# Optimization experiments

Measured on AMD Instinct MI355X. Metric: run time of the kernel, lower is better.

The kernel has to match this reference:

```python
import jax, jax.numpy as jnp
import numpy as np

EPS = 1e-5
AVG_D = 32.0


def setup_inputs() -> dict:
    key = jax.random.key(0)
    ks = jax.random.split(key, 12)
    Ns, Nd, E, D, K = 1_000_000, 100_000, 3_200_000, 16, 2
    Fs, Fd, V = 4, 4, 100_000
    F = Fd + K  # predictor fields
    inp = {}
    inp["Cat_src"] = jax.random.randint(ks[0], (Ns, Fs), 0, V)
    inp["Cat_dst"] = jax.random.randint(ks[1], (Nd, Fd), 0, V)
    inp["src_ids"] = jax.random.randint(ks[2], (E,), 0, Ns)
    inp["dst_ids"] = jax.random.randint(ks[3], (E,), 0, Nd)
    inp["label"] = jax.random.randint(ks[4], (Nd,), 0, 2)
    inp["w"] = jax.random.normal(ks[5], (V, D), dtype=jnp.float32) * 0.05
    inp["W_agg"] = jax.random.normal(ks[6], (K, 12 * D, D), dtype=jnp.float32) * 0.05
    inp["b_agg"] = jnp.zeros((K, D), jnp.float32)
    inp["w_lin"] = jax.random.normal(ks[7], (F * D,), dtype=jnp.float32) * 0.05
    inp["b_lin"] = jnp.zeros((1,), jnp.float32)
    inp["W1"] = jax.random.normal(ks[8], (F * D, 64), dtype=jnp.float32) * 0.05
    inp["b1"] = jnp.zeros((64,), jnp.float32)
    inp["W2"] = jax.random.normal(ks[9], (64, 32), dtype=jnp.float32) * 0.05
    inp["b2"] = jnp.zeros((32,), jnp.float32)
    inp["W3"] = jax.random.normal(ks[10], (32, 1), dtype=jnp.float32) * 0.05
    inp["b3"] = jnp.zeros((1,), jnp.float32)
    return inp


def reference(Cat_src, Cat_dst, src_ids, dst_ids, label, w, W_agg, b_agg,
              w_lin, b_lin, W1, b1, W2, b2, W3, b3):
    Nd = Cat_dst.shape[0]
    # --- node embedding: gather cat fields, RowEmb with modes [mean, max] -> [Ns, K, D]
    emb = w[Cat_src]                                      # [Ns, Fs, D]
    h_src = jnp.stack([emb.mean(1), emb.max(1)], axis=1)  # [Ns, K, D]
    # --- multi-aggregator message passing (copy_u + segment min/max/mean, std via mean of h^2)
    m = h_src[src_ids]                                    # [E, K, D]
    deg = jax.ops.segment_sum(jnp.ones(src_ids.shape, m.dtype), dst_ids, Nd)
    safe = jnp.maximum(deg, 1.0)[:, None, None]
    mean = jax.ops.segment_sum(m, dst_ids, Nd) / safe
    mean2 = jax.ops.segment_sum(m * m, dst_ids, Nd) / safe
    has = (deg > 0)[:, None, None]
    mn = jnp.where(has, jax.ops.segment_min(m, dst_ids, Nd), 0.0)
    mx = jnp.where(has, jax.ops.segment_max(m, dst_ids, Nd), 0.0)
    std = jnp.sqrt(jax.nn.relu(mean2 - mean * mean) + EPS)
    tmp = jnp.concatenate([mean, mn, mx, std], axis=-1)   # [Nd, K, 4D]
    # --- PNA degree scalers: identity / amplification / attenuation
    logd = jnp.log(deg + 1.0)
    log_avg = jnp.log(AVG_D + 1.0)
    amp = (logd / log_avg)[:, None, None]
    att = jnp.where(logd > 0, log_avg / jnp.maximum(logd, EPS), 0.0)[:, None, None]
    scaled = jnp.concatenate([tmp, tmp * amp, tmp * att], axis=-1)  # [Nd, K, 12D]
    mes = jnp.einsum('nkf,kfd->nkd', scaled, W_agg) + b_agg          # [Nd, K, D]
    # --- final block: concat dst cat embeddings with aggregated messages
    x = jnp.concatenate([w[Cat_dst], mes], axis=1)        # [Nd, F, D]
    # --- DeepFM predictor: linear + FM pairwise + deep MLP
    flat = x.reshape(Nd, -1)
    lin = flat @ w_lin + b_lin[0]
    s = x.sum(1)
    fm = 0.5 * ((s * s) - (x * x).sum(1)).sum(-1)
    h = jax.nn.relu(flat @ W1 + b1)
    h = jax.nn.relu(h @ W2 + b2)
    deep = (h @ W3 + b3)[:, 0]
    pred = jax.nn.sigmoid(lin + fm + deep)
    return (pred, label)
```

## Files before the change

### kernel.cpp

```cpp
#include <hip/hip_runtime.h>
#include <math.h>

#define EPSF 1e-5f
#define CAP  88
#define SBH  9
#define MAXSB 256
#define SBCAP 23552
#define TILE 4096
#define XPADS2 104
#define X2PADS 72
#define NPACK 14336

typedef __attribute__((ext_vector_type(8))) short short8;
typedef __attribute__((ext_vector_type(4))) float float4v;

__device__ inline unsigned f2bf_rne(float x) {
    unsigned u = __float_as_uint(x);
    u += 0x7FFF + ((u >> 16) & 1);
    return u >> 16;
}
__device__ inline short bf16_of(float x) { return (short)f2bf_rne(x); }
__device__ inline float bf2f_lo(unsigned hv) { return __uint_as_float(hv << 16); }
__device__ inline float bf2f_hi(unsigned hv) { return __uint_as_float(hv & 0xFFFF0000u); }
__device__ inline float bf2f_s(ushort s) { return __uint_as_float((unsigned)s << 16); }

__global__ __launch_bounds__(256) void setup_all(
    int* sbcursor, int nsb,
    const float* __restrict__ W_agg, const float* __restrict__ W1,
    const float* __restrict__ W2, ushort* __restrict__ wpack,
    const float* __restrict__ w, ushort* __restrict__ wb, int VD, int do_cast)
{
    int bid = blockIdx.x;
    if (bid == 0) {
        int i = threadIdx.x;
        if (i < nsb) sbcursor[i] = i * SBCAP;
        return;
    }
    if (bid == 1) {
        for (int it = threadIdx.x; it < 1792; it += 256) {
            if (it < 768) {
                int t_g = it >> 6; int rem = it & 63;
                int q = rem >> 4, col = rem & 15;
                int kvar = t_g / 6, t = t_g % 6;
                const float* src = W_agg + kvar * 3072 + (t * 32 + q * 8) * 16 + col;
                ushort* dst = wpack + (size_t)it * 8;
#pragma unroll
                for (int j = 0; j < 8; ++j) dst[j] = (ushort)f2bf_rne(src[j * 16]);
            } else if (it < 1536) {
                int i2 = it - 768;
                int t = i2 >> 8; int rem = i2 & 255;
                int q = rem >> 6, col = rem & 63;
                const float* src = W1 + (t * 32 + q * 8) * 64 + col;
                ushort* dst = wpack + 6144 + (size_t)i2 * 8;
#pragma unroll
                for (int j = 0; j < 8; ++j) dst[j] = (ushort)f2bf_rne(src[j * 64]);
            } else {
                int i2 = it - 1536;
                int t = i2 >> 7; int rem = i2 & 127;
                int q = rem >> 5, col = rem & 31;
                const float* src = W2 + (t * 32 + q * 8) * 32 + col;
                ushort* dst = wpack + 12288 + (size_t)i2 * 8;
#pragma unroll
                for (int j = 0; j < 8; ++j) dst[j] = (ushort)f2bf_rne(src[j * 32]);
            }
        }
        return;
    }
    if (!do_cast) return;
    int i4 = ((bid - 2) * 256 + threadIdx.x) * 4;
    if (i4 + 3 < VD) {
        float4 v = *(const float4*)(w + i4);
        ushort4 o;
        o.x = (ushort)f2bf_rne(v.x); o.y = (ushort)f2bf_rne(v.y);
        o.z = (ushort)f2bf_rne(v.z); o.w = (ushort)f2bf_rne(v.w);
        *(ushort4*)(wb + i4) = o;
    } else {
        for (int j = i4; j < VD; ++j) wb[j] = (ushort)f2bf_rne(w[j]);
    }
}

__global__ __launch_bounds__(256) void build_h(
    const int* __restrict__ Cat_src, const ushort* __restrict__ wb,
    unsigned* __restrict__ h, int Ns)
{
    int gid = blockIdx.x * 256 + threadIdx.x;
    int s = gid >> 4;
    if (s >= Ns) return;
    int lane = threadIdx.x & 63;
    int d = lane & 15;
    int c = Cat_src[s * 4 + (d & 3)];
    float vs = 0.f, vm = -INFINITY;
#pragma unroll
    for (int f = 0; f < 4; ++f) {
        int id = __shfl(c, (lane & 48) + f, 64);
        float a = bf2f_s(wb[id * 16 + d]);
        vs += a; vm = fmaxf(vm, a);
    }
    unsigned packed = f2bf_rne(vs * 0.25f) | (f2bf_rne(vm) << 16);
    __builtin_nontemporal_store(packed, &h[s * 16 + d]);
}

__global__ __launch_bounds__(256) void scatter_sb(
    const int* __restrict__ src_ids, const int* __restrict__ dst_ids,
    int* sbcursor, unsigned* __restrict__ pairs1, int E, int nsb)
{
    __shared__ int cnt[MAXSB];
    __shared__ int base[MAXSB];
    int tid = threadIdx.x;
    int t0 = blockIdx.x * TILE;
    for (int i = tid; i < nsb; i += 256) cnt[i] = 0;
    __syncthreads();
    int rank[TILE / 256];
#pragma unroll
    for (int j = 0; j < TILE / 256; ++j) {
        int e = t0 + j * 256 + tid;
        rank[j] = (e < E) ? atomicAdd(&cnt[dst_ids[e] >> SBH], 1) : 0;
    }
    __syncthreads();
    for (int i = tid; i < nsb; i += 256) {
        int c = cnt[i];
        base[i] = c ? atomicAdd(&sbcursor[i], c) : 0;
    }
    __syncthreads();
#pragma unroll
    for (int j = 0; j < TILE / 256; ++j) {
        int e = t0 + j * 256 + tid;
        if (e < E) {
            int d = dst_ids[e];
            int sb = d >> SBH;
            int idx = base[sb] + rank[j];
            if (idx < (sb + 1) * SBCAP)
                pairs1[idx] = ((unsigned)src_ids[e] << 9) | (unsigned)(d & 511);
        }
    }
}

__global__ __launch_bounds__(256) void scatter_fine2(
    const unsigned* __restrict__ pairs1, const int* __restrict__ sbcursor,
    unsigned* __restrict__ pairs2, int* __restrict__ deg, int Nd)
{
    __shared__ int ofs[256];
    int S = blockIdx.x >> 1, half = blockIdx.x & 1;
    int tid = threadIdx.x;
    int sbs = S * SBCAP;
    int sbe = sbcursor[S];
    if (sbe > sbs + SBCAP) sbe = sbs + SBCAP;
    ofs[tid] = 0;
    __syncthreads();
    for (int i = sbs + tid; i < sbe; i += 256) {
        unsigned p = __builtin_nontemporal_load(&pairs1[i]);
        int dl = (int)(p & 511u);
        if ((dl >> 8) == half) {
            int l = dl & 255;
            int sl = atomicAdd(&ofs[l], 1);
            if (sl < CAP)
                pairs2[(size_t)((S << 9) + dl) * CAP + sl] = p >> 9;
        }
    }
    __syncthreads();
    int gdst = (S << 9) + (half << 8) + tid;
    if (gdst < Nd) deg[gdst] = ofs[tid];
}

__device__ inline void emit_stats(float sum0, float sq0, float mn0, float mx0,
                                  float sum1, float sq1, float mn1, float mx1,
                                  int dg, int n, int lane, int sub,
                                  ushort* __restrict__ tmpb)
{
#pragma unroll
    for (int off = 16; off <= 32; off <<= 1) {
        sum0 += __shfl_xor(sum0, off); sq0 += __shfl_xor(sq0, off);
        mn0 = fminf(mn0, __shfl_xor(mn0, off)); mx0 = fmaxf(mx0, __shfl_xor(mx0, off));
        sum1 += __shfl_xor(sum1, off); sq1 += __shfl_xor(sq1, off);
        mn1 = fminf(mn1, __shfl_xor(mn1, off)); mx1 = fmaxf(mx1, __shfl_xor(mx1, off));
    }
    float safe = fmaxf((float)dg, 1.f);
    float r = 1.f / safe;
    bool has = dg > 0;
    float mean0 = sum0 * r, mean1 = sum1 * r;
    float sd0 = sqrtf(fmaxf(sq0 * r - mean0 * mean0, 0.f) + EPSF);
    float sd1 = sqrtf(fmaxf(sq1 * r - mean1 * mean1, 0.f) + EPSF);
    float v0 = (sub == 0) ? mean0 : (sub == 1) ? (has ? mn0 : 0.f)
             : (sub == 2) ? (has ? mx0 : 0.f) : sd0;
    float v1 = (sub == 0) ? mean1 : (sub == 1) ? (has ? mn1 : 0.f)
             : (sub == 2) ? (has ? mx1 : 0.f) : sd1;
    ushort* tp = tmpb + (size_t)n * 128;
    tp[lane] = (ushort)f2bf_rne(v0);
    tp[64 + lane] = (ushort)f2bf_rne(v1);
}

__global__ __launch_bounds__(256) void agg_from_h2(
    const unsigned* __restrict__ h, const int* __restrict__ deg,
    const unsigned* __restrict__ pairs,
    ushort* __restrict__ tmpb, int Nd)
{
    int tid = threadIdx.x;
    int wv = tid >> 6, lane = tid & 63, sub = lane >> 4, d = lane & 15;
    int n = blockIdx.x * 4 + wv;
    if (n >= Nd) return;
    int dg = deg[n];
    int dgc = (dg < CAP) ? dg : CAP;
    const unsigned* pw = pairs + (size_t)n * CAP;

    float sum0 = 0.f, sq0 = 0.f, mn0 = INFINITY, mx0 = -INFINITY;
    float sum1 = 0.f, sq1 = 0.f, mn1 = INFINITY, mx1 = -INFINITY;

    int nfull = dgc >> 5;
    for (int t = 0; t < nfull; ++t) {
        const unsigned* pp = pw + t * 32 + sub;
        unsigned pv[8], hv[8];
#pragma unroll
        for (int j = 0; j < 8; ++j) pv[j] = pp[j * 4];
#pragma unroll
        for (int j = 0; j < 8; ++j) hv[j] = h[pv[j] * 16 + d];
#pragma unroll
        for (int j = 0; j < 8; ++j) {
            float me = bf2f_lo(hv[j]);
            float vm = bf2f_hi(hv[j]);
            sum0 += me; sq0 += me * me;
            mn0 = fminf(mn0, me); mx0 = fmaxf(mx0, me);
            sum1 += vm; sq1 += vm * vm;
            mn1 = fminf(mn1, vm); mx1 = fmaxf(mx1, vm);
        }
    }
    int base = nfull << 5;
    int rem = dgc - base;
    if (rem > 0) {
        int last = dgc - 1;
        unsigned pv[8], hv[8];
#pragma unroll
        for (int j = 0; j < 8; ++j) {
            if (j * 4 < rem) {
                int e = base + j * 4 + sub;
                pv[j] = pw[e < last ? e : last];
            }
        }
#pragma unroll
        for (int j = 0; j < 8; ++j)
            if (j * 4 < rem) hv[j] = h[pv[j] * 16 + d];
#pragma unroll
        for (int j = 0; j < 8; ++j) {
            if (j * 4 < rem) {
                if (base + j * 4 + sub < dgc) {
                    float me = bf2f_lo(hv[j]);
                    float vm = bf2f_hi(hv[j]);
                    sum0 += me; sq0 += me * me;
                    mn0 = fminf(mn0, me); mx0 = fmaxf(mx0, me);
                    sum1 += vm; sq1 += vm * vm;
                    mn1 = fminf(mn1, vm); mx1 = fmaxf(mx1, vm);
                }
            }
        }
    }
    emit_stats(sum0, sq0, mn0, mx0, sum1, sq1, mn1, mx1,
               dg, n, lane, sub, tmpb);
}

__global__ __launch_bounds__(256) void agg_from_w2(
    const int* __restrict__ Cat_src, const float* __restrict__ w,
    const ushort* __restrict__ wb, int use_bf,
    const int* __restrict__ deg, const unsigned* __restrict__ pairs,
    ushort* __restrict__ tmpb, int Nd)
{
    int tid = threadIdx.x;
    int wv = tid >> 6, lane = tid & 63, sub = lane >> 4, d = lane & 15;
    int n = blockIdx.x * 4 + wv;
    if (n >= Nd) return;
    int dg = deg[n];
    int dgc = (dg < CAP) ? dg : CAP;
    const unsigned* pw = pairs + (size_t)n * CAP;

    float sum0 = 0.f, sq0 = 0.f, mn0 = INFINITY, mx0 = -INFINITY;
    float sum1 = 0.f, sq1 = 0.f, mn1 = INFINITY, mx1 = -INFINITY;
    int nt = (dgc + 3) >> 2;
    for (int t = 0; t < nt; ++t) {
        int e4 = t * 4 + sub;
        int ec = (e4 < dgc) ? e4 : (dgc - 1);
        int src = (int)pw[ec];
        int cat = Cat_src[src * 4 + (d & 3)];
        float vs = 0.f, vm = -INFINITY;
        if (use_bf) {
#pragma unroll
            for (int f = 0; f < 4; ++f) {
                int id = __shfl(cat, sub * 16 + f, 64);
                float a = bf2f_s(wb[id * 16 + d]);
                vs += a; vm = fmaxf(vm, a);
            }
        } else {
#pragma unroll
            for (int f = 0; f < 4; ++f) {
                int id = __shfl(cat, sub * 16 + f, 64);
                float a = w[id * 16 + d];
                vs += a; vm = fmaxf(vm, a);
            }
        }
        if (e4 < dgc) {
            float me = vs * 0.25f;
            sum0 += me; sq0 += me * me;
            mn0 = fminf(mn0, me); mx0 = fmaxf(mx0, me);
            sum1 += vm; sq1 += vm * vm;
            mn1 = fminf(mn1, vm); mx1 = fmaxf(mx1, vm);
        }
    }
    emit_stats(sum0, sq0, mn0, mx0, sum1, sq1, mn1, mx1,
               dg, n, lane, sub, tmpb);
}

__global__ __launch_bounds__(256) void finalize_mfma(
    const int* __restrict__ Cat_dst, const int* __restrict__ label,
    const float* __restrict__ w, const ushort* __restrict__ wpack,
    const float* __restrict__ b_agg,
    const float* __restrict__ w_lin, const float* __restrict__ b_lin,
    const float* __restrict__ b1, const float* __restrict__ b2,
    const float* __restrict__ W3, const float* __restrict__ b3,
    const int* __restrict__ deg_arr, const ushort* __restrict__ tmpb,
    float* __restrict__ out, int Nd)
{
    __shared__ __align__(16) ushort sx[4][16 * XPADS2];
    __shared__ __align__(16) ushort sx2[4][16 * X2PADS];
    __shared__ float sdeep[4][16];

    int tid = threadIdx.x;
    int wv = tid >> 6, lane = tid & 63;
    int q = lane >> 4, m = lane & 15;
    int n0 = (blockIdx.x * 4 + wv) * 16;
    int n = n0 + m;
    int nc = (n < Nd) ? n : (Nd - 1);

    ushort* X = sx[wv];
    ushort* X2 = sx2[wv];

    float fdeg = (float)deg_arr[nc];
    float logd = logf(fdeg + 1.f);
    const float logavg = logf(33.0f);
    float amp = logd / logavg;
    float att = (logd > 0.f) ? (logavg / fmaxf(logd, EPSF)) : 0.f;
    float ampr[4], attr[4];
#pragma unroll
    for (int r = 0; r < 4; ++r) {
        ampr[r] = __shfl(amp, q * 4 + r, 64);
        attr[r] = __shfl(att, q * 4 + r, 64);
    }

    const ushort* tpn = tmpb + (size_t)nc * 128;
#pragma unroll
    for (int kvar = 0; kvar < 2; ++kvar) {
        short8 af0 = *(const short8*)(tpn + kvar * 64 + q * 8);
        short8 af1 = *(const short8*)(tpn + kvar * 64 + 32 + q * 8);
        float4v aI = {0.f,0.f,0.f,0.f}, aA = {0.f,0.f,0.f,0.f}, aT = {0.f,0.f,0.f,0.f};
#pragma unroll
        for (int sb = 0; sb < 3; ++sb) {
            short8 b0 = *(const short8*)(wpack +
                (size_t)(((kvar * 6 + sb * 2) * 4 + q) * 16 + m) * 8);
            short8 b1v = *(const short8*)(wpack +
                (size_t)(((kvar * 6 + sb * 2 + 1) * 4 + q) * 16 + m) * 8);
            if (sb == 0) {
                aI = __builtin_amdgcn_mfma_f32_16x16x32_bf16(af0, b0, aI, 0, 0, 0);
                aI = __builtin_amdgcn_mfma_f32_16x16x32_bf16(af1, b1v, aI, 0, 0, 0);
            } else if (sb == 1) {
                aA = __builtin_amdgcn_mfma_f32_16x16x32_bf16(af0, b0, aA, 0, 0, 0);
                aA = __builtin_amdgcn_mfma_f32_16x16x32_bf16(af1, b1v, aA, 0, 0, 0);
            } else {
                aT = __builtin_amdgcn_mfma_f32_16x16x32_bf16(af0, b0, aT, 0, 0, 0);
                aT = __builtin_amdgcn_mfma_f32_16x16x32_bf16(af1, b1v, aT, 0, 0, 0);
            }
        }
        float bias = b_agg[kvar * 16 + m];
#pragma unroll
        for (int r = 0; r < 4; ++r)
            X[(q * 4 + r) * XPADS2 + 64 + kvar * 16 + m] = (ushort)f2bf_rne(
                aI[r] + ampr[r] * aA[r] + attr[r] * aT[r] + bias);
    }
    {
        int nl = lane >> 2, fl = lane & 3;
        int nn = n0 + nl;
        int nnc = (nn < Nd) ? nn : (Nd - 1);
        int cid = Cat_dst[nnc * 4 + fl];
        const float4* R = (const float4*)(w + (size_t)cid * 16);
        float4 r0 = R[0], r1 = R[1], r2 = R[2], r3 = R[3];
        short8 o0, o1;
        o0[0] = bf16_of(r0.x); o0[1] = bf16_of(r0.y);
        o0[2] = bf16_of(r0.z); o0[3] = bf16_of(r0.w);
        o0[4] = bf16_of(r1.x); o0[5] = bf16_of(r1.y);
        o0[6] = bf16_of(r1.z); o0[7] = bf16_of(r1.w);
        o1[0] = bf16_of(r2.x); o1[1] = bf16_of(r2.y);
        o1[2] = bf16_of(r2.z); o1[3] = bf16_of(r2.w);
        o1[4] = bf16_of(r3.x); o1[5] = bf16_of(r3.y);
        o1[6] = bf16_of(r3.z); o1[7] = bf16_of(r3.w);
        ushort* xp = X + nl * XPADS2 + fl * 16;
        *(short8*)(xp) = o0;
        *(short8*)(xp + 8) = o1;
    }
    __syncthreads();

    float lin = 0.f, sq = 0.f;
    float sd[16];
#pragma unroll
    for (int u = 0; u < 16; ++u) sd[u] = 0.f;
    {
        const ushort* xp = X + m * XPADS2 + q * 16;
        const float* wl = w_lin + q * 16;
#pragma unroll
        for (int u = 0; u < 16; ++u) {
            float v = bf2f_s(xp[u]);
            lin += v * wl[u]; sq += v * v; sd[u] += v;
        }
    }
    if (q < 2) {
        const ushort* xp = X + m * XPADS2 + (4 + q) * 16;
        const float* wl = w_lin + (4 + q) * 16;
#pragma unroll
        for (int u = 0; u < 16; ++u) {
            float v = bf2f_s(xp[u]);
            lin += v * wl[u]; sq += v * v; sd[u] += v;
        }
    }
#pragma unroll
    for (int off = 16; off <= 32; off <<= 1) {
        lin += __shfl_xor(lin, off);
        sq  += __shfl_xor(sq, off);
#pragma unroll
        for (int u = 0; u < 16; ++u) sd[u] += __shfl_xor(sd[u], off);
    }
    float fm = 0.f;
#pragma unroll
    for (int u = 0; u < 16; ++u) fm += sd[u] * sd[u];
    fm = 0.5f * (fm - sq);

    short8 xa[3];
#pragma unroll
    for (int t = 0; t < 3; ++t)
        xa[t] = *(const short8*)(X + m * XPADS2 + t * 32 + q * 8);
#pragma unroll
    for (int nt = 0; nt < 4; ++nt) {
        float4v acc = {0.f, 0.f, 0.f, 0.f};
#pragma unroll
        for (int t = 0; t < 3; ++t) {
            short8 bf = *(const short8*)(wpack + 6144 +
                (size_t)((t * 4 + q) * 64 + nt * 16 + m) * 8);
            acc = __builtin_amdgcn_mfma_f32_16x16x32_bf16(xa[t], bf, acc, 0, 0, 0);
        }
        float bb = b1[nt * 16 + m];
#pragma unroll
        for (int r = 0; r < 4; ++r)
            X2[(q * 4 + r) * X2PADS + nt * 16 + m] =
                (ushort)f2bf_rne(fmaxf(acc[r] + bb, 0.f));
    }
    __syncthreads();

    short8 ha[2];
#pragma unroll
    for (int t = 0; t < 2; ++t)
        ha[t] = *(const short8*)(X2 + m * X2PADS + t * 32 + q * 8);
    float dp[4] = {0.f, 0.f, 0.f, 0.f};
#pragma unroll
    for (int nt = 0; nt < 2; ++nt) {
        float4v acc = {0.f, 0.f, 0.f, 0.f};
#pragma unroll
        for (int t = 0; t < 2; ++t) {
            short8 bf = *(const short8*)(wpack + 12288 +
                (size_t)((t * 4 + q) * 32 + nt * 16 + m) * 8);
            acc = __builtin_amdgcn_mfma_f32_16x16x32_bf16(ha[t], bf, acc, 0, 0, 0);
        }
        float bb = b2[nt * 16 + m];
        float w3 = W3[nt * 16 + m];
#pragma unroll
        for (int r = 0; r < 4; ++r)
            dp[r] += fmaxf(acc[r] + bb, 0.f) * w3;
    }
#pragma unroll
    for (int off = 1; off <= 8; off <<= 1) {
#pragma unroll
        for (int r = 0; r < 4; ++r) dp[r] += __shfl_xor(dp[r], off);
    }
    if (m < 4)
        sdeep[wv][q * 4 + m] = (m == 0) ? dp[0] : (m == 1) ? dp[1]
                             : (m == 2) ? dp[2] : dp[3];
    __syncthreads();
    float deep = sdeep[wv][m];

    if (q == 0 && n < Nd) {
        float z = lin + b_lin[0] + fm + deep + b3[0];
        float pred = 1.f / (1.f + expf(-z));
        out[n] = pred;
        out[Nd + n] = (float)label[n];
    }
}

extern "C" void kernel_launch(void* const* d_in, const int* in_sizes, int n_in,
                              void* d_out, int out_size, void* d_ws, size_t ws_size,
                              hipStream_t stream) {
    const int*   Cat_src = (const int*)d_in[0];
    const int*   Cat_dst = (const int*)d_in[1];
    const int*   src_ids = (const int*)d_in[2];
    const int*   dst_ids = (const int*)d_in[3];
    const int*   label   = (const int*)d_in[4];
    const float* w       = (const float*)d_in[5];
    const float* W_agg   = (const float*)d_in[6];
    const float* b_agg   = (const float*)d_in[7];
    const float* w_lin   = (const float*)d_in[8];
    const float* b_lin   = (const float*)d_in[9];
    const float* W1      = (const float*)d_in[10];
    const float* b1      = (const float*)d_in[11];
    const float* W2      = (const float*)d_in[12];
    const float* b2      = (const float*)d_in[13];
    const float* W3      = (const float*)d_in[14];
    const float* b3      = (const float*)d_in[15];

    int E  = in_sizes[2];
    int Nd = in_sizes[4];
    int Ns = in_sizes[0] / 4;
    int VD = in_sizes[5];
    int nsb = (Nd + (1 << SBH) - 1) >> SBH;

    int* sbcursor = (int*)d_ws;
    int* deg      = sbcursor + MAXSB;
    size_t off_p2 = (((size_t)(MAXSB + Nd)) * 4 + 255) & ~(size_t)255;
    unsigned* pairs2 = (unsigned*)((char*)d_ws + off_p2);
    size_t off_u = (off_p2 + (size_t)Nd * CAP * 4 + 255) & ~(size_t)255;
    unsigned* pairs1 = (unsigned*)((char*)d_ws + off_u);
    ushort*   tmpb   = (ushort*)((char*)d_ws + off_u);
    size_t u_p1 = (size_t)nsb * SBCAP * 4;
    size_t u_tm = (size_t)Nd * 256;
    size_t u_bytes = (u_p1 > u_tm) ? u_p1 : u_tm;
    size_t off_w = (off_u + u_bytes + 255) & ~(size_t)255;
    ushort* wpack  = (ushort*)((char*)d_ws + off_w);
    ushort* w_bf16 = wpack + NPACK;
    unsigned* h    = (unsigned*)(w_bf16 + VD);

    size_t need_common = off_w + (size_t)NPACK * 2;
    size_t need_A = need_common + (size_t)VD * 2;
    size_t need_B = need_A + (size_t)Ns * 64;
    int mode = (ws_size >= need_B) ? 2 : (ws_size >= need_A) ? 1 : 0;

    float* out = (float*)d_out;

    int ncb = (mode >= 1) ? (VD / 4 + 255) / 256 : 0;
    hipLaunchKernelGGL(setup_all, dim3(2 + ncb), dim3(256), 0, stream,
                       sbcursor, nsb, W_agg, W1, W2, wpack, w, w_bf16, VD,
                       mode >= 1);
    if (mode == 2) {
        int hb = (int)(((size_t)Ns * 16 + 255) / 256);
        hipLaunchKernelGGL(build_h, dim3(hb), dim3(256), 0, stream,
                           Cat_src, w_bf16, h, Ns);
    }
    hipLaunchKernelGGL(scatter_sb, dim3((E + TILE - 1) / TILE), dim3(256), 0, stream,
                       src_ids, dst_ids, sbcursor, pairs1, E, nsb);
    hipLaunchKernelGGL(scatter_fine2, dim3(nsb * 2), dim3(256), 0, stream,
                       pairs1, sbcursor, pairs2, deg, Nd);
    int nab = (Nd + 3) >> 2;
    if (mode == 2) {
        hipLaunchKernelGGL(agg_from_h2, dim3(nab), dim3(256), 0, stream,
                           h, deg, pairs2, tmpb, Nd);
    } else {
        hipLaunchKernelGGL(agg_from_w2, dim3(nab), dim3(256), 0, stream,
                           Cat_src, w, w_bf16, mode, deg, pairs2, tmpb, Nd);
    }
    hipLaunchKernelGGL(finalize_mfma, dim3((Nd + 63) / 64), dim3(256), 0, stream,
                       Cat_dst, label, w, wpack, b_agg, w_lin, b_lin,
                       b1, b2, W3, b3, deg, tmpb, out, Nd);
}
```

Before: 342.6 us.

## Split fine scatter into segments with global degree atomics; unroll aggregation gather

The fine scatter stage used to run two blocks per destination superblock, and each block walked the whole superblock serially. It now splits each superblock into eight segments handled by separate blocks. Each block ranks its pairs in shared memory and reserves slots per destination with one global atomicAdd on deg, so deg is now zeroed in the setup kernel. The aggregation kernel also processes 64 neighbours per iteration, giving more independent gathers in flight, at the cost of more registers and a neighbour order that is no longer deterministic.

```diff
diff --git a/kernel.cpp b/kernel.cpp
--- a/kernel.cpp
+++ b/kernel.cpp
@@ -7,6 +7,7 @@
 #define MAXSB 256
 #define SBCAP 23552
 #define TILE 4096
+#define SEG  8
 #define XPADS2 104
 #define X2PADS 72
 #define NPACK 14336
@@ -25,18 +26,20 @@
 __device__ inline float bf2f_s(ushort s) { return __uint_as_float((unsigned)s << 16); }
 
 __global__ __launch_bounds__(256) void setup_all(
-    int* sbcursor, int nsb,
+    int* sbcursor, int* deg, int Nd, int nsb,
     const float* __restrict__ W_agg, const float* __restrict__ W1,
     const float* __restrict__ W2, ushort* __restrict__ wpack,
     const float* __restrict__ w, ushort* __restrict__ wb, int VD, int do_cast)
 {
+    int nzc = (Nd + 255) >> 8;
     int bid = blockIdx.x;
-    if (bid == 0) {
-        int i = threadIdx.x;
-        if (i < nsb) sbcursor[i] = i * SBCAP;
+    if (bid < nzc) {
+        int i = bid * 256 + threadIdx.x;
+        if (i < Nd) deg[i] = 0;
+        if (bid == 0 && threadIdx.x < nsb) sbcursor[threadIdx.x] = threadIdx.x * SBCAP;
         return;
     }
-    if (bid == 1) {
+    if (bid == nzc) {
         for (int it = threadIdx.x; it < 1792; it += 256) {
             if (it < 768) {
                 int t_g = it >> 6; int rem = it & 63;
@@ -67,7 +70,7 @@
         return;
     }
     if (!do_cast) return;
-    int i4 = ((bid - 2) * 256 + threadIdx.x) * 4;
+    int i4 = ((bid - nzc - 1) * 256 + threadIdx.x) * 4;
     if (i4 + 3 < VD) {
         float4 v = *(const float4*)(w + i4);
         ushort4 o;
@@ -135,31 +138,56 @@
     }
 }
 
-__global__ __launch_bounds__(256) void scatter_fine2(
+__global__ __launch_bounds__(256) void scatter_fine3(
     const unsigned* __restrict__ pairs1, const int* __restrict__ sbcursor,
-    unsigned* __restrict__ pairs2, int* __restrict__ deg, int Nd)
-{
-    __shared__ int ofs[256];
-    int S = blockIdx.x >> 1, half = blockIdx.x & 1;
+    unsigned* __restrict__ pairs2, int* __restrict__ deg, int Nd, int nsb,
+    int nsbp)
+{
+    __shared__ int cnt[512];
+    __shared__ int base[512];
+    int S = blockIdx.x % nsbp, seg = blockIdx.x / nsbp;
+    if (S >= nsb) return;
     int tid = threadIdx.x;
     int sbs = S * SBCAP;
     int sbe = sbcursor[S];
     if (sbe > sbs + SBCAP) sbe = sbs + SBCAP;
-    ofs[tid] = 0;
-    __syncthreads();
-    for (int i = sbs + tid; i < sbe; i += 256) {
-        unsigned p = __builtin_nontemporal_load(&pairs1[i]);
-        int dl = (int)(p & 511u);
-        if ((dl >> 8) == half) {
-            int l = dl & 255;
-            int sl = atomicAdd(&ofs[l], 1);
-            if (sl < CAP)
-                pairs2[(size_t)((S << 9) + dl) * CAP + sl] = p >> 9;
-        }
-    }
-    __syncthreads();
-    int gdst = (S << 9) + (half << 8) + tid;
-    if (gdst < Nd) deg[gdst] = ofs[tid];
+    int len = sbe - sbs;
+    int per = (len + SEG - 1) / SEG;
+    int s0 = sbs + seg * per;
+    int s1 = s0 + per; if (s1 > sbe) s1 = sbe;
+    cnt[tid] = 0; cnt[tid + 256] = 0;
+    __syncthreads();
+    int rank[12];
+    unsigned pv[12];
+    int nit = (s1 - s0 + 255) >> 8;
+    if (nit > 12) nit = 12;
+    for (int j = 0; j < nit; ++j) {
+        int e = s0 + j * 256 + tid;
+        if (e < s1) {
+            unsigned p = __builtin_nontemporal_load(&pairs1[e]);
+            pv[j] = p;
+            rank[j] = atomicAdd(&cnt[p & 511u], 1);
+        }
+    }
+    __syncthreads();
+#pragma unroll
+    for (int r = 0; r < 2; ++r) {
+        int l = tid + r * 256;
+        int c = cnt[l];
+        int gdst = (S << 9) + l;
+        base[l] = (c && gdst < Nd) ? atomicAdd(&deg[gdst], c) : 0;
+    }
+    __syncthreads();
+    for (int j = 0; j < nit; ++j) {
+        int e = s0 + j * 256 + tid;
+        if (e < s1) {
+            unsigned p = pv[j];
+            int l = (int)(p & 511u);
+            int idx = base[l] + rank[j];
+            if (idx < CAP)
+                pairs2[(size_t)((S << 9) + l) * CAP + idx] = p >> 9;
+        }
+    }
 }
 
 __device__ inline void emit_stats(float sum0, float sq0, float mn0, float mx0,
@@ -189,6 +217,14 @@
     tp[64 + lane] = (ushort)f2bf_rne(v1);
 }
 
+#define ACC8(HV)  do { \
+    float me = bf2f_lo(HV); \
+    float vm = bf2f_hi(HV); \
+    sum0 += me; sq0 += me * me; \
+    mn0 = fminf(mn0, me); mx0 = fmaxf(mx0, me); \
+    sum1 += vm; sq1 += vm * vm; \
+    mn1 = fminf(mn1, vm); mx1 = fmaxf(mx1, vm); } while (0)
+
 __global__ __launch_bounds__(256) void agg_from_h2(
     const unsigned* __restrict__ h, const int* __restrict__ deg,
     const unsigned* __restrict__ pairs,
@@ -205,25 +241,29 @@
     float sum0 = 0.f, sq0 = 0.f, mn0 = INFINITY, mx0 = -INFINITY;
     float sum1 = 0.f, sq1 = 0.f, mn1 = INFINITY, mx1 = -INFINITY;
 
-    int nfull = dgc >> 5;
-    for (int t = 0; t < nfull; ++t) {
-        const unsigned* pp = pw + t * 32 + sub;
+    int t64 = dgc >> 6;
+    for (int t = 0; t < t64; ++t) {
+        const unsigned* pp = pw + t * 64 + sub;
+        unsigned pv[16], hv[16];
+#pragma unroll
+        for (int j = 0; j < 16; ++j) pv[j] = pp[j * 4];
+#pragma unroll
+        for (int j = 0; j < 16; ++j) hv[j] = h[pv[j] * 16 + d];
+#pragma unroll
+        for (int j = 0; j < 16; ++j) ACC8(hv[j]);
+    }
+    int base = t64 << 6;
+    if (dgc & 32) {
+        const unsigned* pp = pw + base + sub;
         unsigned pv[8], hv[8];
 #pragma unroll
         for (int j = 0; j < 8; ++j) pv[j] = pp[j * 4];
 #pragma unroll
         for (int j = 0; j < 8; ++j) hv[j] = h[pv[j] * 16 + d];
 #pragma unroll
-        for (int j = 0; j < 8; ++j) {
-            float me = bf2f_lo(hv[j]);
-            float vm = bf2f_hi(hv[j]);
-            sum0 += me; sq0 += me * me;
-            mn0 = fminf(mn0, me); mx0 = fmaxf(mx0, me);
-            sum1 += vm; sq1 += vm * vm;
-            mn1 = fminf(mn1, vm); mx1 = fmaxf(mx1, vm);
-        }
-    }
-    int base = nfull << 5;
+        for (int j = 0; j < 8; ++j) ACC8(hv[j]);
+        base += 32;
+    }
     int rem = dgc - base;
     if (rem > 0) {
         int last = dgc - 1;
@@ -241,14 +281,7 @@
 #pragma unroll
         for (int j = 0; j < 8; ++j) {
             if (j * 4 < rem) {
-                if (base + j * 4 + sub < dgc) {
-                    float me = bf2f_lo(hv[j]);
-                    float vm = bf2f_hi(hv[j]);
-                    sum0 += me; sq0 += me * me;
-                    mn0 = fminf(mn0, me); mx0 = fmaxf(mx0, me);
-                    sum1 += vm; sq1 += vm * vm;
-                    mn1 = fminf(mn1, vm); mx1 = fmaxf(mx1, vm);
-                }
+                if (base + j * 4 + sub < dgc) ACC8(hv[j]);
             }
         }
     }
@@ -512,6 +545,7 @@
     int Ns = in_sizes[0] / 4;
     int VD = in_sizes[5];
     int nsb = (Nd + (1 << SBH) - 1) >> SBH;
+    int nsbp = (nsb + 7) & ~7;
 
     int* sbcursor = (int*)d_ws;
     int* deg      = sbcursor + MAXSB;
@@ -535,10 +569,11 @@
 
     float* out = (float*)d_out;
 
+    int nzc = (Nd + 255) >> 8;
     int ncb = (mode >= 1) ? (VD / 4 + 255) / 256 : 0;
-    hipLaunchKernelGGL(setup_all, dim3(2 + ncb), dim3(256), 0, stream,
-                       sbcursor, nsb, W_agg, W1, W2, wpack, w, w_bf16, VD,
-                       mode >= 1);
+    hipLaunchKernelGGL(setup_all, dim3(nzc + 1 + ncb), dim3(256), 0, stream,
+                       sbcursor, deg, Nd, nsb, W_agg, W1, W2, wpack,
+                       w, w_bf16, VD, mode >= 1);
     if (mode == 2) {
         int hb = (int)(((size_t)Ns * 16 + 255) / 256);
         hipLaunchKernelGGL(build_h, dim3(hb), dim3(256), 0, stream,
@@ -546,8 +581,8 @@
     }
     hipLaunchKernelGGL(scatter_sb, dim3((E + TILE - 1) / TILE), dim3(256), 0, stream,
                        src_ids, dst_ids, sbcursor, pairs1, E, nsb);
-    hipLaunchKernelGGL(scatter_fine2, dim3(nsb * 2), dim3(256), 0, stream,
-                       pairs1, sbcursor, pairs2, deg, Nd);
+    hipLaunchKernelGGL(scatter_fine3, dim3(nsbp * SEG), dim3(256), 0, stream,
+                       pairs1, sbcursor, pairs2, deg, Nd, nsb, nsbp);
     int nab = (Nd + 3) >> 2;
     if (mode == 2) {
         hipLaunchKernelGGL(agg_from_h2, dim3(nab), dim3(256), 0, stream,
```

Result: faster. 316.7 us (-7.6%).
